# Kernel optimization log

Measured on AMD Instinct MI355X. Metric: run time of the kernel, lower is better.

Reference implementation:

```python
import jax, jax.numpy as jnp
import numpy as np

ENC_DIM = 1024
EMB_DIM = 256
K = 8192          # codebook size
COMMIT = 0.25
LN_EPS = 1e-5


def _ln(x, g, b):
    m = jnp.mean(x, axis=-1, keepdims=True)
    v = jnp.mean(jnp.square(x - m), axis=-1, keepdims=True)
    return (x - m) * jax.lax.rsqrt(v + LN_EPS) * g + b


def _mlp(x, W1, b1, g1, be1, W2, b2, g2, be2):
    # two feed_forward blocks: Linear -> ReLU -> LayerNorm
    x = _ln(jax.nn.relu(x @ W1 + b1), g1, be1)
    x = _ln(jax.nn.relu(x @ W2 + b2), g2, be2)
    return x


def setup_inputs() -> dict:
    key = jax.random.key(0)
    ks = jax.random.split(key, 10)
    d = ENC_DIM
    s = 1.0 / np.sqrt(d)
    inp = {"x": jax.random.normal(ks[0], (4, 2048, d), dtype=jnp.float32)}
    # encoder MLP (2 blocks)
    inp["We1"] = jax.random.uniform(ks[1], (d, d), jnp.float32, -s, s)
    inp["be1"] = jnp.zeros((d,), jnp.float32)
    inp["ge1"] = jnp.ones((d,), jnp.float32)
    inp["bne1"] = jnp.zeros((d,), jnp.float32)
    inp["We2"] = jax.random.uniform(ks[2], (d, d), jnp.float32, -s, s)
    inp["be2"] = jnp.zeros((d,), jnp.float32)
    inp["ge2"] = jnp.ones((d,), jnp.float32)
    inp["bne2"] = jnp.zeros((d,), jnp.float32)
    # decoder MLP (2 blocks)
    inp["Wd1"] = jax.random.uniform(ks[3], (d, d), jnp.float32, -s, s)
    inp["bd1"] = jnp.zeros((d,), jnp.float32)
    inp["gd1"] = jnp.ones((d,), jnp.float32)
    inp["bnd1"] = jnp.zeros((d,), jnp.float32)
    inp["Wd2"] = jax.random.uniform(ks[4], (d, d), jnp.float32, -s, s)
    inp["bd2"] = jnp.zeros((d,), jnp.float32)
    inp["gd2"] = jnp.ones((d,), jnp.float32)
    inp["bnd2"] = jnp.zeros((d,), jnp.float32)
    # codebook, init uniform(-1/K, 1/K)
    inp["codebook"] = jax.random.uniform(ks[5], (K, EMB_DIM), jnp.float32, -1.0 / K, 1.0 / K)
    return inp


def reference(x, We1, be1, ge1, bne1, We2, be2, ge2, bne2,
              Wd1, bd1, gd1, bnd1, Wd2, bd2, gd2, bnd2, codebook):
    bs, seq_len, d = x.shape
    z = _mlp(x, We1, be1, ge1, bne1, We2, be2, ge2, bne2)

    # ---- VectorQuantizer ----
    zg = z.reshape(bs, seq_len, -1, EMB_DIM)              # (b, s, g, e)
    flat = zg.reshape(-1, EMB_DIM)                        # (N, e)
    # pairwise squared distances to codebook: (N, K)
    dist = (jnp.sum(flat * flat, axis=1, keepdims=True)
            + jnp.sum(codebook * codebook, axis=1)
            - 2.0 * flat @ codebook.T)
    idx = jnp.argmin(dist, axis=1)                        # (N,)
    quantized = jnp.take(codebook, idx, axis=0).reshape(zg.shape)

    e_latent = jnp.mean(jnp.square(jax.lax.stop_gradient(quantized) - zg))
    q_latent = jnp.mean(jnp.square(quantized - jax.lax.stop_gradient(zg)))
    loss = q_latent + COMMIT * e_latent

    # straight-through estimator
    quantized = zg + jax.lax.stop_gradient(quantized - zg)
    quantized = quantized.reshape(bs, seq_len, d)

    # perplexity from code usage histogram
    n = flat.shape[0]
    counts = jnp.zeros((K,), x.dtype).at[idx].add(1.0)
    avg_probs = counts / n
    perplexity = jnp.exp(-jnp.sum(avg_probs * jnp.log(avg_probs + 1e-10)))

    out = _mlp(quantized, Wd1, bd1, gd1, bnd1, Wd2, bd2, gd2, bnd2)
    return (out, loss, perplexity)
```

## Files before the change

kernel.cpp:

```cpp
#include <hip/hip_runtime.h>
#include <stdint.h>


typedef short bf16x8 __attribute__((ext_vector_type(8)));
typedef float f32x4 __attribute__((ext_vector_type(4)));

__device__ __forceinline__ void gl2lds16(const void* g, void* l) {
  __builtin_amdgcn_global_load_lds(
      (const __attribute__((address_space(1))) void*)g,
      (__attribute__((address_space(3))) void*)l, 16, 0, 0);
}

__device__ __forceinline__ float bf2f(unsigned short u) {
  return __uint_as_float(((unsigned)u) << 16);
}
__device__ __forceinline__ unsigned short f2bf(float f) {
  unsigned x = __float_as_uint(f);
  unsigned r = (x + 0x7fffu + ((x >> 16) & 1u)) >> 16;
  return (unsigned short)r;
}
__device__ __forceinline__ unsigned long long packScore(float s, int code) {
  unsigned u = __float_as_uint(s);
  u = (u & 0x80000000u) ? ~u : (u | 0x80000000u);
  return ((unsigned long long)u << 32) | (unsigned)code;
}
__device__ __forceinline__ unsigned long long shflxor_u64(unsigned long long v, int m) {
  union { unsigned long long u; int i[2]; } a;
  a.u = v;
  a.i[0] = __shfl_xor(a.i[0], m);
  a.i[1] = __shfl_xor(a.i[1], m);
  return a.u;
}

__global__ __launch_bounds__(256)
void cast_bf16(const float* __restrict__ X, unsigned short* __restrict__ Y, int n4) {
  int i = blockIdx.x * 256 + threadIdx.x;
  if (i < n4) {
    float4 v = ((const float4*)X)[i];
    ushort4 o = make_ushort4(f2bf(v.x), f2bf(v.y), f2bf(v.z), f2bf(v.w));
    ((ushort4*)Y)[i] = o;
  }
}

__global__ __launch_bounds__(256)
void transpose_cast(const float* __restrict__ W, unsigned short* __restrict__ Wt, int D) {
  __shared__ float s[32][33];
  int tx = threadIdx.x & 31, ty = threadIdx.x >> 5;
  int bx = blockIdx.x, by = blockIdx.y;
#pragma unroll
  for (int p = 0; p < 4; p++) {
    int r = by * 32 + ty + p * 8, c = bx * 32 + tx;
    s[ty + p * 8][tx] = W[(size_t)r * D + c];
  }
  __syncthreads();
#pragma unroll
  for (int p = 0; p < 4; p++) {
    int r = bx * 32 + ty + p * 8, c = by * 32 + tx;
    Wt[(size_t)r * D + c] = f2bf(s[tx][ty + p * 8]);
  }
}

__global__ __launch_bounds__(256)
void code_norms(const float* __restrict__ cb, float* __restrict__ cn) {
  int row = blockIdx.x * 4 + (threadIdx.x >> 6);
  int lane = threadIdx.x & 63;
  float4 v = ((const float4*)(cb + (size_t)row * 256))[lane];
  float s = v.x * v.x + v.y * v.y + v.z * v.z + v.w * v.w;
#pragma unroll
  for (int off = 32; off > 0; off >>= 1) s += __shfl_down(s, off);
  if (lane == 0) cn[row] = s;
}

__global__ __launch_bounds__(256, 2)
void gemm_bias_relu(const unsigned short* __restrict__ A, const unsigned short* __restrict__ Bt,
                    const float* __restrict__ bias, unsigned short* __restrict__ C,
                    int M, int N, int K) {
  __shared__ unsigned short As[128 * 64];
  __shared__ unsigned short Bs[128 * 64];
  const int t = threadIdx.x;
  const int wv = t >> 6, lane = t & 63;
  const int wm = wv >> 1, wn = wv & 1;
  const int quad = lane >> 4, l15 = lane & 15;
  const int row0 = blockIdx.y * 128, col0 = blockIdx.x * 128;
  const int rsub = lane >> 3;
  const int dchunk = (lane & 7) ^ rsub;

  f32x4 acc[4][4];
#pragma unroll
  for (int i = 0; i < 4; i++)
#pragma unroll
    for (int j = 0; j < 4; j++) acc[i][j] = (f32x4){0.f, 0.f, 0.f, 0.f};

  for (int k0 = 0; k0 < K; k0 += 64) {
#pragma unroll
    for (int j = 0; j < 4; j++) {
      int slab = j * 4 + wv;
      int row = slab * 8 + rsub;
      gl2lds16(A + (size_t)(row0 + row) * K + k0 + dchunk * 8, As + slab * 512);
      gl2lds16(Bt + (size_t)(col0 + row) * K + k0 + dchunk * 8, Bs + slab * 512);
    }
    __syncthreads();
#pragma unroll
    for (int kk = 0; kk < 2; kk++) {
      bf16x8 af[4], bfr[4];
#pragma unroll
      for (int mt = 0; mt < 4; mt++) {
        int row = wm * 64 + mt * 16 + l15;
        af[mt] = *(const bf16x8*)(As + row * 64 + (((kk * 4 + quad) ^ (l15 & 7)) * 8));
      }
#pragma unroll
      for (int nt = 0; nt < 4; nt++) {
        int row = wn * 64 + nt * 16 + l15;
        bfr[nt] = *(const bf16x8*)(Bs + row * 64 + (((kk * 4 + quad) ^ (l15 & 7)) * 8));
      }
#pragma unroll
      for (int mt = 0; mt < 4; mt++)
#pragma unroll
        for (int nt = 0; nt < 4; nt++)
          acc[mt][nt] = __builtin_amdgcn_mfma_f32_16x16x32_bf16(af[mt], bfr[nt], acc[mt][nt], 0, 0, 0);
    }
    __syncthreads();
  }
#pragma unroll
  for (int mt = 0; mt < 4; mt++) {
#pragma unroll
    for (int nt = 0; nt < 4; nt++) {
      int col = col0 + wn * 64 + nt * 16 + l15;
      float b = bias[col];
#pragma unroll
      for (int r = 0; r < 4; r++) {
        int row = row0 + wm * 64 + mt * 16 + quad * 4 + r;
        float v = acc[mt][nt][r] + b;
        C[(size_t)row * N + col] = f2bf(v > 0.f ? v : 0.f);
      }
    }
  }
}

__global__ __launch_bounds__(256)
void ln_kernel(const unsigned short* __restrict__ X, const float* __restrict__ g,
               const float* __restrict__ b, unsigned short* __restrict__ obf,
               float* __restrict__ of32) {
  const int row = blockIdx.x, t = threadIdx.x;
  ushort4 u = ((const ushort4*)(X + (size_t)row * 1024))[t];
  float4 v = make_float4(bf2f(u.x), bf2f(u.y), bf2f(u.z), bf2f(u.w));
  float s = v.x + v.y + v.z + v.w;
  float ss = v.x * v.x + v.y * v.y + v.z * v.z + v.w * v.w;
#pragma unroll
  for (int off = 32; off > 0; off >>= 1) {
    s += __shfl_down(s, off);
    ss += __shfl_down(ss, off);
  }
  __shared__ float rs[4], rss[4];
  const int wave = t >> 6, lane = t & 63;
  if (lane == 0) { rs[wave] = s; rss[wave] = ss; }
  __syncthreads();
  float S = rs[0] + rs[1] + rs[2] + rs[3];
  float SS = rss[0] + rss[1] + rss[2] + rss[3];
  float m = S * (1.0f / 1024.0f);
  float var = SS * (1.0f / 1024.0f) - m * m;
  float rstd = 1.0f / sqrtf(var + 1e-5f);
  float4 gv = ((const float4*)g)[t];
  float4 bv = ((const float4*)b)[t];
  float4 o;
  o.x = (v.x - m) * rstd * gv.x + bv.x;
  o.y = (v.y - m) * rstd * gv.y + bv.y;
  o.z = (v.z - m) * rstd * gv.z + bv.z;
  o.w = (v.w - m) * rstd * gv.w + bv.w;
  if (obf) {
    ushort4 q = make_ushort4(f2bf(o.x), f2bf(o.y), f2bf(o.z), f2bf(o.w));
    ((ushort4*)(obf + (size_t)row * 1024))[t] = q;
  } else {
    ((float4*)(of32 + (size_t)row * 1024))[t] = o;
  }
}

__global__ __launch_bounds__(256, 2)
void vq_dist(const unsigned short* __restrict__ Z, const unsigned short* __restrict__ Cb,
             const float* __restrict__ cnorm, unsigned long long* __restrict__ bestg) {
  __shared__ unsigned short Bs[2][64 * 256];
  __shared__ unsigned long long runmin[64];
  const int t = threadIdx.x;
  const int wv = t >> 6, lane = t & 63;
  const int quad = lane >> 4, l15 = lane & 15;
  const int row0 = blockIdx.x * 64;

  if (t < 64) runmin[t] = ~0ull;

  bf16x8 zf[4][8];
#pragma unroll
  for (int mt = 0; mt < 4; mt++)
#pragma unroll
    for (int ks = 0; ks < 8; ks++)
      zf[mt][ks] = *(const bf16x8*)(Z + (size_t)(row0 + mt * 16 + l15) * 256 + ks * 32 + quad * 8);

  float msc[4][4];
  int mcd[4][4];
#pragma unroll
  for (int mt = 0; mt < 4; mt++)
#pragma unroll
    for (int r = 0; r < 4; r++) { msc[mt][r] = 3.4e38f; mcd[mt][r] = 0; }

  const int dcode = lane >> 5;
  const int dgr = lane & 31;
  const int slot = wv * 16 + l15;
  const int rxor = l15 & 7;

#pragma unroll
  for (int j = 0; j < 8; j++) {
    int slab = wv * 8 + j;
    int sl = slab * 2 + dcode;
    gl2lds16(Cb + (size_t)sl * 256 + ((dgr ^ (sl & 7)) * 8), &Bs[0][slab * 512]);
  }
  float cn_cur = cnorm[slot];
  float cn_prev = 3.4e38f;
  f32x4 pacc[4];
#pragma unroll
  for (int mt = 0; mt < 4; mt++) pacc[mt] = (f32x4){0.f, 0.f, 0.f, 0.f};

  for (int ch = 0; ch < 128; ch++) {
    const int cur = ch & 1;
    __builtin_amdgcn_s_waitcnt(0x3F70);

    {
      const int cb2 = ((ch + 1) & 127) * 64;
#pragma unroll
      for (int j = 0; j < 8; j++) {
        int slab = wv * 8 + j;
        int sl = slab * 2 + dcode;
        gl2lds16(Cb + (size_t)(cb2 + sl) * 256 + ((dgr ^ (sl & 7)) * 8),
                 &Bs[cur ^ 1][slab * 512]);
      }
    }
    float cn_next = cnorm[(((ch + 1) & 127) * 64) + slot];

    bf16x8 lbuf[3];
    lbuf[0] = *(const bf16x8*)(&Bs[cur][slot * 256 + ((quad ^ rxor) * 8)]);
    lbuf[1] = *(const bf16x8*)(&Bs[cur][slot * 256 + (((4 + quad) ^ rxor) * 8)]);

    {
      int code = (ch - 1) * 64 + slot;
#pragma unroll
      for (int mt = 0; mt < 4; mt++)
#pragma unroll
        for (int r = 0; r < 4; r++) {
          float sc = cn_prev - 2.0f * pacc[mt][r];
          if (sc < msc[mt][r]) { msc[mt][r] = sc; mcd[mt][r] = code; }
        }
    }

#pragma unroll
    for (int ks = 0; ks < 8; ks++) {
      if (ks + 2 < 8)
        lbuf[(ks + 2) % 3] =
            *(const bf16x8*)(&Bs[cur][slot * 256 + ((((ks + 2) * 4 + quad) ^ rxor) * 8)]);
      bf16x8 lb = lbuf[ks % 3];
      if (ks == 0) {
        const f32x4 z4 = (f32x4){0.f, 0.f, 0.f, 0.f};
#pragma unroll
        for (int mt = 0; mt < 4; mt++)
          pacc[mt] = __builtin_amdgcn_mfma_f32_16x16x32_bf16(zf[mt][0], lb, z4, 0, 0, 0);
      } else {
#pragma unroll
        for (int mt = 0; mt < 4; mt++)
          pacc[mt] = __builtin_amdgcn_mfma_f32_16x16x32_bf16(zf[mt][ks], lb, pacc[mt], 0, 0, 0);
      }
    }
    cn_prev = cn_cur;
    cn_cur = cn_next;
  }
  {
    int code = 127 * 64 + slot;
#pragma unroll
    for (int mt = 0; mt < 4; mt++)
#pragma unroll
      for (int r = 0; r < 4; r++) {
        float sc = cn_prev - 2.0f * pacc[mt][r];
        if (sc < msc[mt][r]) { msc[mt][r] = sc; mcd[mt][r] = code; }
      }
  }

  __syncthreads();
#pragma unroll
  for (int mt = 0; mt < 4; mt++) {
#pragma unroll
    for (int r = 0; r < 4; r++) {
      unsigned long long bp = packScore(msc[mt][r], mcd[mt][r]);
#pragma unroll
      for (int m = 1; m < 16; m <<= 1) {
        unsigned long long o = shflxor_u64(bp, m);
        bp = o < bp ? o : bp;
      }
      if (l15 == 0) atomicMin(&runmin[mt * 16 + quad * 4 + r], bp);
    }
  }
  __syncthreads();
  if (t < 64) bestg[row0 + t] = runmin[t];
}

__global__ __launch_bounds__(256)
void vq_gather(const unsigned long long* __restrict__ bestg, const float* __restrict__ cb,
               const unsigned short* __restrict__ zb, unsigned short* __restrict__ qb,
               int* __restrict__ counts, float* __restrict__ lpart) {
  const int wave = threadIdx.x >> 6;
  const int g = blockIdx.x * 4 + wave;
  const int lane = threadIdx.x & 63;
  const int idx = (int)(bestg[g] & 0xFFFFFFFFull);
  float4 c = ((const float4*)(cb + (size_t)idx * 256))[lane];
  ushort4 q = make_ushort4(f2bf(c.x), f2bf(c.y), f2bf(c.z), f2bf(c.w));
  ((ushort4*)(qb + (size_t)g * 256))[lane] = q;
  ushort4 z = ((const ushort4*)(zb + (size_t)g * 256))[lane];
  float dx = c.x - bf2f(z.x), dy = c.y - bf2f(z.y);
  float dz = c.z - bf2f(z.z), dw = c.w - bf2f(z.w);
  float p = dx * dx + dy * dy + dz * dz + dw * dw;
#pragma unroll
  for (int off = 32; off > 0; off >>= 1) p += __shfl_down(p, off);
  __shared__ float sp[4];
  if (lane == 0) {
    sp[wave] = p;
    atomicAdd(&counts[idx], 1);
  }
  __syncthreads();
  if (threadIdx.x == 0) lpart[blockIdx.x] = sp[0] + sp[1] + sp[2] + sp[3];
}

__global__ __launch_bounds__(256)
void finalize(const int* __restrict__ counts, const float* __restrict__ lpart,
              float* __restrict__ out2) {
  const int t = threadIdx.x;
  double h = 0.0, l = 0.0;
  for (int i = t; i < 8192; i += 256) {
    double pr = (double)counts[i] * (1.0 / 32768.0);
    h += pr * log(pr + 1e-10);
    l += (double)lpart[i];
  }
  __shared__ double sh[256], sl[256];
  sh[t] = h;
  sl[t] = l;
  __syncthreads();
  for (int w = 128; w > 0; w >>= 1) {
    if (t < w) { sh[t] += sh[t + w]; sl[t] += sl[t + w]; }
    __syncthreads();
  }
  if (t == 0) {
    out2[0] = (float)(1.25 * sl[0] * (1.0 / 8388608.0));
    out2[1] = (float)exp(-sh[0]);
  }
}

extern "C" void kernel_launch(void* const* d_in, const int* in_sizes, int n_in,
                              void* d_out, int out_size, void* d_ws, size_t ws_size,
                              hipStream_t stream) {
  const float* x = (const float*)d_in[0];
  const float* We1 = (const float*)d_in[1];
  const float* be1 = (const float*)d_in[2];
  const float* ge1 = (const float*)d_in[3];
  const float* bne1 = (const float*)d_in[4];
  const float* We2 = (const float*)d_in[5];
  const float* be2 = (const float*)d_in[6];
  const float* ge2 = (const float*)d_in[7];
  const float* bne2 = (const float*)d_in[8];
  const float* Wd1 = (const float*)d_in[9];
  const float* bd1 = (const float*)d_in[10];
  const float* gd1 = (const float*)d_in[11];
  const float* bnd1 = (const float*)d_in[12];
  const float* Wd2 = (const float*)d_in[13];
  const float* bd2 = (const float*)d_in[14];
  const float* gd2 = (const float*)d_in[15];
  const float* bnd2 = (const float*)d_in[16];
  const float* codebook = (const float*)d_in[17];
  float* out = (float*)d_out;

  char* w = (char*)d_ws;
  auto alloc = [&](size_t bytes) -> char* {
    char* p = w;
    w += (bytes + 255) & ~(size_t)255;
    return p;
  };
  unsigned short* xb = (unsigned short*)alloc((size_t)8192 * 1024 * 2);
  unsigned short* wt0 = (unsigned short*)alloc((size_t)1024 * 1024 * 2);
  unsigned short* wt1 = (unsigned short*)alloc((size_t)1024 * 1024 * 2);
  unsigned short* wt2 = (unsigned short*)alloc((size_t)1024 * 1024 * 2);
  unsigned short* wt3 = (unsigned short*)alloc((size_t)1024 * 1024 * 2);
  unsigned short* cbb = (unsigned short*)alloc((size_t)8192 * 256 * 2);
  float* cnorm = (float*)alloc((size_t)8192 * 4);
  unsigned short* act = (unsigned short*)alloc((size_t)8192 * 1024 * 2);
  unsigned short* yb = (unsigned short*)alloc((size_t)8192 * 1024 * 2);
  unsigned short* zb = (unsigned short*)alloc((size_t)8192 * 1024 * 2);
  unsigned short* qb = (unsigned short*)alloc((size_t)8192 * 1024 * 2);
  unsigned long long* best = (unsigned long long*)alloc((size_t)32768 * 8);
  int* counts = (int*)alloc((size_t)8192 * 4);
  float* lpart = (float*)alloc((size_t)8192 * 4);

  hipMemsetAsync(counts, 0, (size_t)8192 * 4, stream);

  cast_bf16<<<(2097152 + 255) / 256, 256, 0, stream>>>(x, xb, 2097152);
  dim3 tg(32, 32);
  transpose_cast<<<tg, 256, 0, stream>>>(We1, wt0, 1024);
  transpose_cast<<<tg, 256, 0, stream>>>(We2, wt1, 1024);
  transpose_cast<<<tg, 256, 0, stream>>>(Wd1, wt2, 1024);
  transpose_cast<<<tg, 256, 0, stream>>>(Wd2, wt3, 1024);
  cast_bf16<<<(524288 + 255) / 256, 256, 0, stream>>>(codebook, cbb, 524288);
  code_norms<<<2048, 256, 0, stream>>>(codebook, cnorm);

  dim3 gg(8, 64);
  gemm_bias_relu<<<gg, 256, 0, stream>>>(xb, wt0, be1, act, 8192, 1024, 1024);
  ln_kernel<<<8192, 256, 0, stream>>>(act, ge1, bne1, yb, nullptr);
  gemm_bias_relu<<<gg, 256, 0, stream>>>(yb, wt1, be2, act, 8192, 1024, 1024);
  ln_kernel<<<8192, 256, 0, stream>>>(act, ge2, bne2, zb, nullptr);
  vq_dist<<<512, 256, 0, stream>>>(zb, cbb, cnorm, best);
  vq_gather<<<8192, 256, 0, stream>>>(best, codebook, zb, qb, counts, lpart);
  gemm_bias_relu<<<gg, 256, 0, stream>>>(qb, wt2, bd1, act, 8192, 1024, 1024);
  ln_kernel<<<8192, 256, 0, stream>>>(act, gd1, bnd1, yb, nullptr);
  gemm_bias_relu<<<gg, 256, 0, stream>>>(yb, wt3, bd2, act, 8192, 1024, 1024);
  ln_kernel<<<8192, 256, 0, stream>>>(act, gd2, bnd2, nullptr, out);

  finalize<<<1, 256, 0, stream>>>(counts, lpart, out + 8388608);
}
```

Before: 465.1 us.

## Process 128 codes per chunk, streaming second half directly from global into registers

The VQ argmin kernel now handles 128 codebook entries per iteration instead of 64. The first 64 still go through the double-buffered LDS path, and the second 64 are loaded straight from global memory into registers with a 3-deep prefetch. This halves the loop trip count and the LDS traffic per code, and doubles the MFMA work per chunk to better hide latency. The cost is more registers (two accumulator sets plus a global prefetch buffer) and uncoalesced, L2-dependent global reads of the codebook.

```diff
diff --git a/kernel.cpp b/kernel.cpp
--- a/kernel.cpp
+++ b/kernel.cpp
@@ -206,24 +206,36 @@
   const int slot = wv * 16 + l15;
   const int rxor = l15 & 7;
 
+  const unsigned short* gbase = Cb + (size_t)(64 + slot) * 256 + quad * 8;
+
 #pragma unroll
   for (int j = 0; j < 8; j++) {
     int slab = wv * 8 + j;
     int sl = slab * 2 + dcode;
     gl2lds16(Cb + (size_t)sl * 256 + ((dgr ^ (sl & 7)) * 8), &Bs[0][slab * 512]);
   }
-  float cn_cur = cnorm[slot];
-  float cn_prev = 3.4e38f;
-  f32x4 pacc[4];
-#pragma unroll
-  for (int mt = 0; mt < 4; mt++) pacc[mt] = (f32x4){0.f, 0.f, 0.f, 0.f};
-
-  for (int ch = 0; ch < 128; ch++) {
+  float cn0c = cnorm[slot];
+  float cn1c = cnorm[64 + slot];
+  float cn0p = 3.4e38f, cn1p = 3.4e38f;
+  bf16x8 gbuf[4];
+  gbuf[0] = *(const bf16x8*)(gbase + 0 * 32);
+  gbuf[1] = *(const bf16x8*)(gbase + 1 * 32);
+  gbuf[2] = *(const bf16x8*)(gbase + 2 * 32);
+
+  f32x4 pacc[4][2];
+#pragma unroll
+  for (int mt = 0; mt < 4; mt++) {
+    pacc[mt][0] = (f32x4){0.f, 0.f, 0.f, 0.f};
+    pacc[mt][1] = (f32x4){0.f, 0.f, 0.f, 0.f};
+  }
+
+  for (int ch = 0; ch < 64; ch++) {
     const int cur = ch & 1;
-    __builtin_amdgcn_s_waitcnt(0x3F70);
+    __builtin_amdgcn_s_waitcnt(0x3F73);
+    __builtin_amdgcn_sched_barrier(0);
 
     {
-      const int cb2 = ((ch + 1) & 127) * 64;
+      const int cb2 = ((ch + 1) & 63) * 128;
 #pragma unroll
       for (int j = 0; j < 8; j++) {
         int slab = wv * 8 + j;
@@ -232,21 +244,26 @@
                  &Bs[cur ^ 1][slab * 512]);
       }
     }
-    float cn_next = cnorm[(((ch + 1) & 127) * 64) + slot];
+    float cn0n = cnorm[(((ch + 1) & 63) * 128) + slot];
+    float cn1n = cnorm[(((ch + 1) & 63) * 128) + 64 + slot];
 
     bf16x8 lbuf[3];
     lbuf[0] = *(const bf16x8*)(&Bs[cur][slot * 256 + ((quad ^ rxor) * 8)]);
     lbuf[1] = *(const bf16x8*)(&Bs[cur][slot * 256 + (((4 + quad) ^ rxor) * 8)]);
 
     {
-      int code = (ch - 1) * 64 + slot;
-#pragma unroll
-      for (int mt = 0; mt < 4; mt++)
-#pragma unroll
-        for (int r = 0; r < 4; r++) {
-          float sc = cn_prev - 2.0f * pacc[mt][r];
-          if (sc < msc[mt][r]) { msc[mt][r] = sc; mcd[mt][r] = code; }
-        }
+      int code0 = (ch - 1) * 128 + slot;
+#pragma unroll
+      for (int p = 0; p < 2; p++) {
+        float cn = p == 0 ? cn0p : cn1p;
+#pragma unroll
+        for (int mt = 0; mt < 4; mt++)
+#pragma unroll
+          for (int r = 0; r < 4; r++) {
+            float sc = cn - 2.0f * pacc[mt][p][r];
+            if (sc < msc[mt][r]) { msc[mt][r] = sc; mcd[mt][r] = code0 + p * 64; }
+          }
+      }
     }
 
 #pragma unroll
@@ -254,30 +271,44 @@
       if (ks + 2 < 8)
         lbuf[(ks + 2) % 3] =
             *(const bf16x8*)(&Bs[cur][slot * 256 + ((((ks + 2) * 4 + quad) ^ rxor) * 8)]);
+      {
+        const int ksn = (ks + 3) & 7;
+        const int chn = (ks + 3 > 7) ? ((ch + 1) & 63) : ch;
+        gbuf[(ks + 3) & 3] = *(const bf16x8*)(gbase + (size_t)chn * 32768 + ksn * 32);
+      }
       bf16x8 lb = lbuf[ks % 3];
+      bf16x8 gb = gbuf[ks & 3];
       if (ks == 0) {
         const f32x4 z4 = (f32x4){0.f, 0.f, 0.f, 0.f};
 #pragma unroll
-        for (int mt = 0; mt < 4; mt++)
-          pacc[mt] = __builtin_amdgcn_mfma_f32_16x16x32_bf16(zf[mt][0], lb, z4, 0, 0, 0);
+        for (int mt = 0; mt < 4; mt++) {
+          pacc[mt][0] = __builtin_amdgcn_mfma_f32_16x16x32_bf16(zf[mt][0], lb, z4, 0, 0, 0);
+          pacc[mt][1] = __builtin_amdgcn_mfma_f32_16x16x32_bf16(zf[mt][0], gb, z4, 0, 0, 0);
+        }
       } else {
 #pragma unroll
-        for (int mt = 0; mt < 4; mt++)
-          pacc[mt] = __builtin_amdgcn_mfma_f32_16x16x32_bf16(zf[mt][ks], lb, pacc[mt], 0, 0, 0);
-      }
-    }
-    cn_prev = cn_cur;
-    cn_cur = cn_next;
+        for (int mt = 0; mt < 4; mt++) {
+          pacc[mt][0] = __builtin_amdgcn_mfma_f32_16x16x32_bf16(zf[mt][ks], lb, pacc[mt][0], 0, 0, 0);
+          pacc[mt][1] = __builtin_amdgcn_mfma_f32_16x16x32_bf16(zf[mt][ks], gb, pacc[mt][1], 0, 0, 0);
+        }
+      }
+    }
+    cn0p = cn0c; cn1p = cn1c;
+    cn0c = cn0n; cn1c = cn1n;
   }
   {
-    int code = 127 * 64 + slot;
-#pragma unroll
-    for (int mt = 0; mt < 4; mt++)
-#pragma unroll
-      for (int r = 0; r < 4; r++) {
-        float sc = cn_prev - 2.0f * pacc[mt][r];
-        if (sc < msc[mt][r]) { msc[mt][r] = sc; mcd[mt][r] = code; }
-      }
+    int code0 = 63 * 128 + slot;
+#pragma unroll
+    for (int p = 0; p < 2; p++) {
+      float cn = p == 0 ? cn0p : cn1p;
+#pragma unroll
+      for (int mt = 0; mt < 4; mt++)
+#pragma unroll
+        for (int r = 0; r < 4; r++) {
+          float sc = cn - 2.0f * pacc[mt][p][r];
+          if (sc < msc[mt][r]) { msc[mt][r] = sc; mcd[mt][r] = code0 + p * 64; }
+        }
+    }
   }
 
   __syncthreads();
```

Result: slower. 635.5 us (+36.6%).
